# Kernel optimization log

Hardware: AMD Instinct MI355X
Metric: run time of the kernel (lower is better)

The kernel has to match this reference:

```python
import jax, jax.numpy as jnp
import numpy as np

D_MODEL, HEADS, D_FF = 1024, 16, 4096
D_K = D_MODEL // HEADS
EPS = 1e-5


def layer_norm(x, g, b):
    mu = jnp.mean(x, axis=-1, keepdims=True)
    var = jnp.mean((x - mu) ** 2, axis=-1, keepdims=True)
    return (x - mu) * jax.lax.rsqrt(var + EPS) * g + b


def setup_inputs() -> dict:
    key = jax.random.key(0)
    ks = jax.random.split(key, 16)
    B, S = 2, 2048
    s = 0.02
    return {
        "src": jax.random.normal(ks[0], (B, S, D_MODEL), jnp.float32),
        "corr": jax.random.normal(ks[1], (B, S, S), jnp.float32),
        "pos": jax.random.normal(ks[2], (B, S, D_MODEL), jnp.float32),
        "Wq": jax.random.normal(ks[3], (D_MODEL, D_MODEL), jnp.float32) * s,
        "bq": jnp.zeros((D_MODEL,), jnp.float32),
        "Wk": jax.random.normal(ks[4], (D_MODEL, D_MODEL), jnp.float32) * s,
        "bk": jnp.zeros((D_MODEL,), jnp.float32),
        "Wv": jax.random.normal(ks[5], (D_MODEL, D_MODEL), jnp.float32) * s,
        "bv": jnp.zeros((D_MODEL,), jnp.float32),
        "Wo": jax.random.normal(ks[6], (D_MODEL, D_MODEL), jnp.float32) * s,
        "bo": jnp.zeros((D_MODEL,), jnp.float32),
        "W1": jax.random.normal(ks[7], (D_MODEL, D_FF), jnp.float32) * s,
        "b1": jnp.zeros((D_FF,), jnp.float32),
        "W2": jax.random.normal(ks[8], (D_FF, D_MODEL), jnp.float32) * s,
        "b2": jnp.zeros((D_MODEL,), jnp.float32),
        "g1": jnp.ones((D_MODEL,), jnp.float32),
        "be1": jnp.zeros((D_MODEL,), jnp.float32),
        "g2": jnp.ones((D_MODEL,), jnp.float32),
        "be2": jnp.zeros((D_MODEL,), jnp.float32),
    }


def reference(src, corr, pos, Wq, bq, Wk, bk, Wv, bv, Wo, bo, W1, b1, W2, b2, g1, be1, g2, be2):
    B, S, _ = src.shape
    qk_in = src + pos  # with_pos_embed for q and k; value uses raw src
    # QKV projections -> [B, H, S, d_k]
    def split_heads(x):
        return x.reshape(B, S, HEADS, D_K).transpose(0, 2, 1, 3)
    q = split_heads(qk_in @ Wq + bq)
    k = split_heads(qk_in @ Wk + bk)
    v = split_heads(src @ Wv + bv)
    # scores [B, H, S, S] with additive correlation bias before softmax
    scores = jnp.einsum("bhqd,bhkd->bhqk", q, k) / jnp.sqrt(jnp.float32(D_K))
    scores = scores + corr[:, None, :, :]
    attn = jax.nn.softmax(scores, axis=-1)
    ctx = jnp.einsum("bhqk,bhkd->bhqd", attn, v)
    concat = ctx.transpose(0, 2, 1, 3).reshape(B, S, D_MODEL)
    attn_out = concat @ Wo + bo
    # post-norm residual blocks (dropout = identity in eval)
    x = layer_norm(src + attn_out, g1, be1)
    ffn = jax.nn.relu(x @ W1 + b1) @ W2 + b2
    x = layer_norm(x + ffn, g2, be2)
    return x
```

## Files before the change

### kernel.cpp

```cpp
#include <hip/hip_runtime.h>
#include <hip/hip_bf16.h>

#define S_LEN  2048
#define BATCH  2
#define DMODEL 1024
#define NHEAD  16
#define DHEAD  64
#define DFF    4096
#define NTOK   (BATCH * S_LEN)
#define QKVLD  3072

typedef __attribute__((ext_vector_type(8))) short short8;
typedef __attribute__((ext_vector_type(4))) short short4v;
typedef __attribute__((ext_vector_type(4))) float f32x4;

__device__ __forceinline__ short f2bs(float f) {
  __hip_bfloat16 h = __float2bfloat16(f);
  short s;
  __builtin_memcpy(&s, &h, sizeof(short));
  return s;
}

__device__ __forceinline__ float bs2f(short s) {
  unsigned u = ((unsigned)(unsigned short)s) << 16;
  float f;
  __builtin_memcpy(&f, &u, sizeof(float));
  return f;
}

__device__ __forceinline__ f32x4 mfma16(short8 a, short8 b, f32x4 c) {
  return __builtin_amdgcn_mfma_f32_16x16x32_bf16(a, b, c, 0, 0, 0);
}

__device__ __forceinline__ void load_lds16(const short* g, short* l) {
  __builtin_amdgcn_global_load_lds(
      (const __attribute__((address_space(1))) void*)g,
      (__attribute__((address_space(3))) void*)l, 16, 0, 0);
}

__global__ void transpose_cast(const float* __restrict__ in, short* __restrict__ out,
                               int R, int C, float scale) {
  __shared__ float tile[32][33];
  const int c0 = blockIdx.x * 32, r0 = blockIdx.y * 32;
  const int tx = threadIdx.x, ty = threadIdx.y;
#pragma unroll
  for (int i = 0; i < 32; i += 8)
    tile[ty + i][tx] = in[(size_t)(r0 + ty + i) * C + c0 + tx];
  __syncthreads();
#pragma unroll
  for (int i = 0; i < 32; i += 8)
    out[(size_t)(c0 + ty + i) * R + r0 + tx] = f2bs(tile[tx][ty + i] * scale);
}

__global__ __launch_bounds__(256) void transpose_bf16(
    const short* __restrict__ in, short* __restrict__ out, int R, int LDin) {
  __shared__ __attribute__((aligned(16))) short tile[64][72];
  const int c0 = blockIdx.x * 64, r0 = blockIdx.y * 64;
#pragma unroll
  for (int i = 0; i < 2; i++) {
    const int idx = threadIdx.x + 256 * i;
    const int rr = idx >> 3, cc8 = (idx & 7) * 8;
    *(int4*)(&tile[rr][cc8]) = *(const int4*)(in + (size_t)(r0 + rr) * LDin + c0 + cc8);
  }
  __syncthreads();
#pragma unroll
  for (int i = 0; i < 2; i++) {
    const int idx = threadIdx.x + 256 * i;
    const int rr = idx >> 3, cc8 = (idx & 7) * 8;
    short8 v;
#pragma unroll
    for (int j = 0; j < 8; j++) v[j] = tile[cc8 + j][rr];
    *(short8*)(out + (size_t)(c0 + rr) * R + r0 + cc8) = v;
  }
}

__global__ void concat_bias(const float* __restrict__ bq, const float* __restrict__ bk,
                            const float* __restrict__ bv, float* __restrict__ bqkv) {
  const int i = blockIdx.x * 256 + threadIdx.x;
  float v;
  if (i < DMODEL) v = bq[i] * 0.125f;
  else if (i < 2 * DMODEL) v = bk[i - DMODEL];
  else v = bv[i - 2 * DMODEL];
  bqkv[i] = v;
}

__global__ void prep_tokens(const float* __restrict__ src, const float* __restrict__ pos,
                            short* __restrict__ qkb, short* __restrict__ srcb) {
  const int i = (blockIdx.x * blockDim.x + threadIdx.x) * 4;
  float4 s = *(const float4*)(src + i);
  float4 p = *(const float4*)(pos + i);
  short4v q4 = {f2bs(s.x + p.x), f2bs(s.y + p.y), f2bs(s.z + p.z), f2bs(s.w + p.w)};
  short4v s4 = {f2bs(s.x), f2bs(s.y), f2bs(s.z), f2bs(s.w)};
  *(short4v*)(qkb + i) = q4;
  *(short4v*)(srcb + i) = s4;
}

__global__ void prep_corr(const float* __restrict__ corr, short* __restrict__ corrb) {
  const size_t i = ((size_t)blockIdx.x * 256 + threadIdx.x) * 4;
  float4 c = *(const float4*)(corr + i);
  short4v o = {f2bs(c.x), f2bs(c.y), f2bs(c.z), f2bs(c.w)};
  *(short4v*)(corrb + i) = o;
}

template <int RELU, int OUT_BF16>
__global__ __launch_bounds__(256) void gemm_bt(
    const short* __restrict__ A0, const short* __restrict__ A1,
    const short* __restrict__ Bt, const float* __restrict__ bias,
    float* __restrict__ Cf, short* __restrict__ Cb,
    int M, int N, int K, int splitcol) {
  __shared__ __attribute__((aligned(16))) short As[128 * 32];
  __shared__ __attribute__((aligned(16))) short Bs[128 * 32];

  const int tid = threadIdx.x;
  const int wave = tid >> 6, lane = tid & 63;
  const int lm = lane & 15, lq = lane >> 4;
  const int row0 = blockIdx.y * 128, col0 = blockIdx.x * 128;
  const int wr = (wave >> 1) * 64, wc = (wave & 1) * 64;

  const short* A = (col0 < splitcol) ? A0 : A1;
  const short* ag = A + (size_t)(row0 + wave * 32 + (lane >> 2)) * K + (lane & 3) * 8;
  const short* bg = Bt + (size_t)(col0 + wave * 32 + (lane >> 2)) * K + (lane & 3) * 8;
  short* asl = &As[wave * 32 * 32];
  short* bsl = &Bs[wave * 32 * 32];

  f32x4 acc[4][4];
#pragma unroll
  for (int i = 0; i < 4; i++)
#pragma unroll
    for (int j = 0; j < 4; j++) acc[i][j] = (f32x4){0.f, 0.f, 0.f, 0.f};

  for (int k0 = 0; k0 < K; k0 += 32) {
    load_lds16(ag + k0, asl);
    load_lds16(ag + (size_t)16 * K + k0, asl + 16 * 32);
    load_lds16(bg + k0, bsl);
    load_lds16(bg + (size_t)16 * K + k0, bsl + 16 * 32);
    __syncthreads();

    short8 af[4], bfr[4];
#pragma unroll
    for (int i = 0; i < 4; i++)
      af[i] = *(const short8*)(&As[(wr + 16 * i + lm) * 32 + lq * 8]);
#pragma unroll
    for (int j = 0; j < 4; j++)
      bfr[j] = *(const short8*)(&Bs[(wc + 16 * j + lm) * 32 + lq * 8]);
#pragma unroll
    for (int i = 0; i < 4; i++)
#pragma unroll
      for (int j = 0; j < 4; j++) acc[i][j] = mfma16(af[i], bfr[j], acc[i][j]);
    __syncthreads();
  }

#pragma unroll
  for (int i = 0; i < 4; i++) {
#pragma unroll
    for (int j = 0; j < 4; j++) {
      const int col = col0 + wc + 16 * j + lm;
      const float bs = bias[col];
#pragma unroll
      for (int r = 0; r < 4; r++) {
        const int row = row0 + wr + 16 * i + lq * 4 + r;
        float v = acc[i][j][r] + bs;
        if (RELU) v = fmaxf(v, 0.f);
        if (OUT_BF16)
          Cb[(size_t)row * N + col] = f2bs(v);
        else
          Cf[(size_t)row * N + col] = v;
      }
    }
  }
}

__global__ __launch_bounds__(256) void gemm_bt_part(
    const short* __restrict__ A, const short* __restrict__ Bt,
    float* __restrict__ Cf, int M, int N, int K, int Kslice) {
  __shared__ __attribute__((aligned(16))) short As[128 * 32];
  __shared__ __attribute__((aligned(16))) short Bs[128 * 32];

  const int tid = threadIdx.x;
  const int wave = tid >> 6, lane = tid & 63;
  const int lm = lane & 15, lq = lane >> 4;
  const int row0 = blockIdx.y * 128, col0 = blockIdx.x * 128;
  const int kbase = blockIdx.z * Kslice;
  const int wr = (wave >> 1) * 64, wc = (wave & 1) * 64;
  Cf += (size_t)blockIdx.z * M * N;

  const short* ag = A + (size_t)(row0 + wave * 32 + (lane >> 2)) * K + (lane & 3) * 8;
  const short* bg = Bt + (size_t)(col0 + wave * 32 + (lane >> 2)) * K + (lane & 3) * 8;
  short* asl = &As[wave * 32 * 32];
  short* bsl = &Bs[wave * 32 * 32];

  f32x4 acc[4][4];
#pragma unroll
  for (int i = 0; i < 4; i++)
#pragma unroll
    for (int j = 0; j < 4; j++) acc[i][j] = (f32x4){0.f, 0.f, 0.f, 0.f};

  for (int k0 = kbase; k0 < kbase + Kslice; k0 += 32) {
    load_lds16(ag + k0, asl);
    load_lds16(ag + (size_t)16 * K + k0, asl + 16 * 32);
    load_lds16(bg + k0, bsl);
    load_lds16(bg + (size_t)16 * K + k0, bsl + 16 * 32);
    __syncthreads();

    short8 af[4], bfr[4];
#pragma unroll
    for (int i = 0; i < 4; i++)
      af[i] = *(const short8*)(&As[(wr + 16 * i + lm) * 32 + lq * 8]);
#pragma unroll
    for (int j = 0; j < 4; j++)
      bfr[j] = *(const short8*)(&Bs[(wc + 16 * j + lm) * 32 + lq * 8]);
#pragma unroll
    for (int i = 0; i < 4; i++)
#pragma unroll
      for (int j = 0; j < 4; j++) acc[i][j] = mfma16(af[i], bfr[j], acc[i][j]);
    __syncthreads();
  }

#pragma unroll
  for (int i = 0; i < 4; i++) {
#pragma unroll
    for (int j = 0; j < 4; j++) {
      const int col = col0 + wc + 16 * j + lm;
#pragma unroll
      for (int r = 0; r < 4; r++) {
        const int row = row0 + wr + 16 * i + lq * 4 + r;
        Cf[(size_t)row * N + col] = acc[i][j][r];
      }
    }
  }
}

__global__ __launch_bounds__(256, 4) void attn_kernel(
    const short* __restrict__ QKV,
    const short* __restrict__ VT,
    const short* __restrict__ corrb,
    float* __restrict__ Op,
    float* __restrict__ lp) {
  const int h = blockIdx.x, qtile = blockIdx.y;
  const int b = blockIdx.z >> 1, split = blockIdx.z & 1;
  const int koff = split * (S_LEN / 2);
  const int tid = threadIdx.x;
  const int wave = tid >> 6, lane = tid & 63;
  const int lm = lane & 15, lq = lane >> 4;
  const int qb = qtile * 128 + wave * 32;
  const int fx = lm & 7;

  __shared__ __attribute__((aligned(16))) short Ks[64 * 64];
  __shared__ __attribute__((aligned(16))) short Vs[64 * 64];
  __shared__ __attribute__((aligned(16))) short Ps[4 * 32 * 64];

  const short* q0 = QKV + (size_t)(b * S_LEN + qb + lm) * QKVLD + h * DHEAD;
  const short* q1 = q0 + (size_t)16 * QKVLD;
  const short8 qA0 = *(const short8*)(q0 + lq * 8);
  const short8 qA1 = *(const short8*)(q0 + lq * 8 + 32);
  const short8 qB0 = *(const short8*)(q1 + lq * 8);
  const short8 qB1 = *(const short8*)(q1 + lq * 8 + 32);

  f32x4 oA[4], oB[4];
#pragma unroll
  for (int t = 0; t < 4; t++) {
    oA[t] = (f32x4){0.f, 0.f, 0.f, 0.f};
    oB[t] = (f32x4){0.f, 0.f, 0.f, 0.f};
  }
  f32x4 laccA = (f32x4){0.f, 0.f, 0.f, 0.f};
  f32x4 laccB = (f32x4){0.f, 0.f, 0.f, 0.f};

  const short* Kp = QKV + (size_t)(b * S_LEN) * QKVLD + DMODEL + h * DHEAD;
  const short* Vp = VT + (size_t)(h * DHEAD) * NTOK + b * S_LEN;
  const short* c0 = corrb + (size_t)(b * S_LEN + qb + lm) * S_LEN;
  const short* c1 = c0 + (size_t)16 * S_LEN;

  const int sr = tid >> 2;
  const int su = tid & 3;
  const int sw0 = (su ^ (sr & 7)) * 8;
  const int sw1 = ((su + 4) ^ (sr & 7)) * 8;

  for (int kt = koff; kt < koff + S_LEN / 2; kt += 64) {
    const short* kr = Kp + (size_t)(kt + sr) * QKVLD + su * 8;
    const short* vr = Vp + (size_t)sr * NTOK + kt + su * 8;
    *(int4*)(&Ks[sr * 64 + sw0]) = *(const int4*)kr;
    *(int4*)(&Ks[sr * 64 + sw1]) = *(const int4*)(kr + 32);
    *(int4*)(&Vs[sr * 64 + sw0]) = *(const int4*)vr;
    *(int4*)(&Vs[sr * 64 + sw1]) = *(const int4*)(vr + 32);
    __syncthreads();

    f32x4 svA[4], svB[4];
#pragma unroll
    for (int t = 0; t < 4; t++) {
      const int rb = (t * 16 + lm) * 64;
      const short8 kf0 = *(const short8*)(&Ks[rb + (lq ^ fx) * 8]);
      const short8 kf1 = *(const short8*)(&Ks[rb + ((lq + 4) ^ fx) * 8]);
      f32x4 a = (f32x4){0.f, 0.f, 0.f, 0.f};
      a = mfma16(kf0, qA0, a);
      a = mfma16(kf1, qA1, a);
      svA[t] = a;
      f32x4 c = (f32x4){0.f, 0.f, 0.f, 0.f};
      c = mfma16(kf0, qB0, c);
      c = mfma16(kf1, qB1, c);
      svB[t] = c;
    }

#pragma unroll
    for (int t = 0; t < 4; t++) {
      const short4v crA = *(const short4v*)(c0 + kt + t * 16 + lq * 4);
      const short4v crB = *(const short4v*)(c1 + kt + t * 16 + lq * 4);
#pragma unroll
      for (int r = 0; r < 4; r++) {
        svA[t][r] = __expf(svA[t][r] + bs2f(crA[r]));
        svB[t][r] = __expf(svB[t][r] + bs2f(crB[r]));
      }
      laccA += svA[t];
      laccB += svB[t];
      short4v pA = {f2bs(svA[t][0]), f2bs(svA[t][1]), f2bs(svA[t][2]), f2bs(svA[t][3])};
      short4v pB = {f2bs(svB[t][0]), f2bs(svB[t][1]), f2bs(svB[t][2]), f2bs(svB[t][3])};
      const int pu = ((2 * t + (lq >> 1)) ^ fx) * 8 + (lq & 1) * 4;
      *(short4v*)(&Ps[wave * 2048 + lm * 64 + pu]) = pA;
      *(short4v*)(&Ps[wave * 2048 + (16 + lm) * 64 + pu]) = pB;
    }

    const int pbA = wave * 2048 + lm * 64;
    const int pbB = pbA + 16 * 64;
    const short8 pA0 = *(const short8*)(&Ps[pbA + (lq ^ fx) * 8]);
    const short8 pA1 = *(const short8*)(&Ps[pbA + ((lq + 4) ^ fx) * 8]);
    const short8 pB0 = *(const short8*)(&Ps[pbB + (lq ^ fx) * 8]);
    const short8 pB1 = *(const short8*)(&Ps[pbB + ((lq + 4) ^ fx) * 8]);
#pragma unroll
    for (int t = 0; t < 4; t++) {
      const int rb = (t * 16 + lm) * 64;
      const short8 vf0 = *(const short8*)(&Vs[rb + (lq ^ fx) * 8]);
      const short8 vf1 = *(const short8*)(&Vs[rb + ((lq + 4) ^ fx) * 8]);
      oA[t] = mfma16(vf0, pA0, oA[t]);
      oA[t] = mfma16(vf1, pA1, oA[t]);
      oB[t] = mfma16(vf0, pB0, oB[t]);
      oB[t] = mfma16(vf1, pB1, oB[t]);
    }
    __syncthreads();
  }

  float lA = laccA[0] + laccA[1] + laccA[2] + laccA[3];
  float lB = laccB[0] + laccB[1] + laccB[2] + laccB[3];
  lA += __shfl_xor(lA, 16);
  lA += __shfl_xor(lA, 32);
  lB += __shfl_xor(lB, 16);
  lB += __shfl_xor(lB, 32);
  if (lq == 0) {
    lp[((size_t)split * NTOK + b * S_LEN + qb + lm) * NHEAD + h] = lA;
    lp[((size_t)split * NTOK + b * S_LEN + qb + 16 + lm) * NHEAD + h] = lB;
  }
  float* opA = Op + (size_t)split * NTOK * DMODEL +
               (size_t)(b * S_LEN + qb + lm) * DMODEL + h * DHEAD;
  float* opB = opA + (size_t)16 * DMODEL;
#pragma unroll
  for (int t = 0; t < 4; t++) {
    *(f32x4*)(opA + t * 16 + lq * 4) = oA[t];
    *(f32x4*)(opB + t * 16 + lq * 4) = oB[t];
  }
}

__global__ __launch_bounds__(256) void combine_ctx(
    const float* __restrict__ Op, const float* __restrict__ lp,
    short* __restrict__ ctx) {
  const size_t idx = ((size_t)blockIdx.x * 256 + threadIdx.x) * 4;
  const int token = (int)(idx >> 10);
  const int d = (int)(idx & 1023);
  const int h = d >> 6;
  const f32x4 o0 = *(const f32x4*)(Op + idx);
  const f32x4 o1 = *(const f32x4*)(Op + (size_t)NTOK * DMODEL + idx);
  const float l0 = lp[(size_t)token * NHEAD + h];
  const float l1 = lp[((size_t)NTOK + token) * NHEAD + h];
  const float inv = 1.0f / (l0 + l1);
  short4v ov = {f2bs((o0[0] + o1[0]) * inv), f2bs((o0[1] + o1[1]) * inv),
                f2bs((o0[2] + o1[2]) * inv), f2bs((o0[3] + o1[3]) * inv)};
  *(short4v*)(ctx + idx) = ov;
}

__global__ __launch_bounds__(256) void residual_ln3(
    const float* __restrict__ xa, const float* __restrict__ p0,
    const float* __restrict__ p1, const float* __restrict__ bias,
    const float* __restrict__ g, const float* __restrict__ be,
    float* __restrict__ outf, short* __restrict__ outb) {
  const int row = blockIdx.x;
  const int t = threadIdx.x;
  const size_t base = (size_t)row * DMODEL + t * 4;
  float4 a = *(const float4*)(xa + base);
  f32x4 q0 = *(const f32x4*)(p0 + base);
  f32x4 q1 = *(const f32x4*)(p1 + base);
  f32x4 bb = *(const f32x4*)(bias + t * 4);
  const float v0 = a.x + q0[0] + q1[0] + bb[0];
  const float v1 = a.y + q0[1] + q1[1] + bb[1];
  const float v2 = a.z + q0[2] + q1[2] + bb[2];
  const float v3 = a.w + q0[3] + q1[3] + bb[3];
  float sum = v0 + v1 + v2 + v3;
  float sq = v0 * v0 + v1 * v1 + v2 * v2 + v3 * v3;
#pragma unroll
  for (int off = 1; off < 64; off <<= 1) {
    sum += __shfl_xor(sum, off);
    sq += __shfl_xor(sq, off);
  }
  __shared__ float ssum[4], ssq[4];
  const int wave = t >> 6;
  if ((t & 63) == 0) { ssum[wave] = sum; ssq[wave] = sq; }
  __syncthreads();
  sum = ssum[0] + ssum[1] + ssum[2] + ssum[3];
  sq = ssq[0] + ssq[1] + ssq[2] + ssq[3];
  const float mean = sum * (1.0f / DMODEL);
  const float var = sq * (1.0f / DMODEL) - mean * mean;
  const float rstd = rsqrtf(var + 1e-5f);
  float4 gv = *(const float4*)(g + t * 4);
  float4 bv = *(const float4*)(be + t * 4);
  const float o0 = (v0 - mean) * rstd * gv.x + bv.x;
  const float o1 = (v1 - mean) * rstd * gv.y + bv.y;
  const float o2 = (v2 - mean) * rstd * gv.z + bv.z;
  const float o3 = (v3 - mean) * rstd * gv.w + bv.w;
  if (outf) {
    float4 ov = {o0, o1, o2, o3};
    *(float4*)(outf + base) = ov;
  }
  if (outb) {
    short4v ob = {f2bs(o0), f2bs(o1), f2bs(o2), f2bs(o3)};
    *(short4v*)(outb + base) = ob;
  }
}

extern "C" void kernel_launch(void* const* d_in, const int* in_sizes, int n_in,
                              void* d_out, int out_size, void* d_ws, size_t ws_size,
                              hipStream_t stream) {
  const float* src = (const float*)d_in[0];
  const float* corr = (const float*)d_in[1];
  const float* pos = (const float*)d_in[2];
  const float* Wq = (const float*)d_in[3];
  const float* bq = (const float*)d_in[4];
  const float* Wk = (const float*)d_in[5];
  const float* bk = (const float*)d_in[6];
  const float* Wv = (const float*)d_in[7];
  const float* bv = (const float*)d_in[8];
  const float* Wo = (const float*)d_in[9];
  const float* bo = (const float*)d_in[10];
  const float* W1 = (const float*)d_in[11];
  const float* b1 = (const float*)d_in[12];
  const float* W2 = (const float*)d_in[13];
  const float* b2 = (const float*)d_in[14];
  const float* g1 = (const float*)d_in[15];
  const float* be1 = (const float*)d_in[16];
  const float* g2 = (const float*)d_in[17];
  const float* be2 = (const float*)d_in[18];
  float* out = (float*)d_out;

  char* ws = (char*)d_ws;
  size_t off = 0;
  auto alloc = [&](size_t bytes) {
    char* p = ws + off;
    off += (bytes + 255) & ~(size_t)255;
    return p;
  };
  short* WqkvT = (short*)alloc((size_t)QKVLD * DMODEL * 2);
  short* WoT = (short*)alloc((size_t)DMODEL * DMODEL * 2);
  short* W1T = (short*)alloc((size_t)DFF * DMODEL * 2);
  short* W2T = (short*)alloc((size_t)DMODEL * DFF * 2);
  float* bqkv = (float*)alloc((size_t)QKVLD * 4);
  short* qkb = (short*)alloc((size_t)NTOK * DMODEL * 2);
  short* srcb = (short*)alloc((size_t)NTOK * DMODEL * 2);
  short* QKVb = (short*)alloc((size_t)NTOK * QKVLD * 2);
  short* VTt = (short*)alloc((size_t)DMODEL * NTOK * 2);
  short* corrb = (short*)alloc((size_t)BATCH * S_LEN * S_LEN * 2);
  short* ctxb = (short*)alloc((size_t)NTOK * DMODEL * 2);
  float* lp = (float*)alloc((size_t)2 * NTOK * NHEAD * 4);
  float* Pp = (float*)alloc((size_t)2 * NTOK * DMODEL * 4);
  float* x1f = (float*)alloc((size_t)NTOK * DMODEL * 4);
  short* x1b = (short*)alloc((size_t)NTOK * DMODEL * 2);
  short* Hb = (short*)alloc((size_t)NTOK * DFF * 2);
  float* Op = (float*)Hb;

  const dim3 tb(32, 8);
  transpose_cast<<<dim3(32, 32), tb, 0, stream>>>(Wq, WqkvT, DMODEL, DMODEL, 0.125f);
  transpose_cast<<<dim3(32, 32), tb, 0, stream>>>(Wk, WqkvT + (size_t)DMODEL * DMODEL,
                                                  DMODEL, DMODEL, 1.0f);
  transpose_cast<<<dim3(32, 32), tb, 0, stream>>>(Wv, WqkvT + (size_t)2 * DMODEL * DMODEL,
                                                  DMODEL, DMODEL, 1.0f);
  transpose_cast<<<dim3(32, 32), tb, 0, stream>>>(Wo, WoT, DMODEL, DMODEL, 1.0f);
  transpose_cast<<<dim3(128, 32), tb, 0, stream>>>(W1, W1T, DMODEL, DFF, 1.0f);
  transpose_cast<<<dim3(32, 128), tb, 0, stream>>>(W2, W2T, DFF, DMODEL, 1.0f);
  concat_bias<<<QKVLD / 256, 256, 0, stream>>>(bq, bk, bv, bqkv);

  prep_tokens<<<(NTOK * DMODEL) / (256 * 4), 256, 0, stream>>>(src, pos, qkb, srcb);
  prep_corr<<<(BATCH * S_LEN * S_LEN) / (256 * 4), 256, 0, stream>>>(corr, corrb);

  gemm_bt<0, 1><<<dim3(QKVLD / 128, NTOK / 128), 256, 0, stream>>>(
      qkb, srcb, WqkvT, bqkv, nullptr, QKVb, NTOK, QKVLD, DMODEL, 2048);

  transpose_bf16<<<dim3(DMODEL / 64, NTOK / 64), 256, 0, stream>>>(
      QKVb + 2048, VTt, NTOK, QKVLD);

  attn_kernel<<<dim3(NHEAD, S_LEN / 128, BATCH * 2), 256, 0, stream>>>(
      QKVb, VTt, corrb, Op, lp);
  combine_ctx<<<(NTOK * DMODEL) / (256 * 4), 256, 0, stream>>>(Op, lp, ctxb);

  gemm_bt_part<<<dim3(DMODEL / 128, NTOK / 128, 2), 256, 0, stream>>>(
      ctxb, WoT, Pp, NTOK, DMODEL, DMODEL, DMODEL / 2);

  residual_ln3<<<NTOK, 256, 0, stream>>>(src, Pp, Pp + (size_t)NTOK * DMODEL,
                                         bo, g1, be1, x1f, x1b);

  gemm_bt<1, 1><<<dim3(DFF / 128, NTOK / 128), 256, 0, stream>>>(
      x1b, x1b, W1T, b1, nullptr, Hb, NTOK, DFF, DMODEL, 1 << 30);

  gemm_bt_part<<<dim3(DMODEL / 128, NTOK / 128, 2), 256, 0, stream>>>(
      Hb, W2T, Pp, NTOK, DMODEL, DFF, DFF / 2);

  residual_ln3<<<NTOK, 256, 0, stream>>>(x1f, Pp, Pp + (size_t)NTOK * DMODEL,
                                         b2, g2, be2, out, nullptr);
}
```

Baseline: 489.3 us.

## Read fp32 corr directly in attention, split keys four ways, use direct-to-LDS loads

Removes the separate corr-to-bf16 conversion pass and has the attention kernel read the fp32 correlation bias directly, prefetching it before the QK MFMAs. The key dimension is now split four ways instead of two for more blocks, and K/V tiles are staged with direct global-to-LDS loads using an XOR-swizzled layout. MFMA sections get raised wave priority, and the occupancy hint goes from 4 to 5. Partial outputs are placed in the Pp buffer, and the combine kernel sums four partials, which adds more partial-result traffic.

```diff
diff --git a/kernel.cpp b/kernel.cpp
--- a/kernel.cpp
+++ b/kernel.cpp
@@ -9,6 +9,7 @@
 #define DFF    4096
 #define NTOK   (BATCH * S_LEN)
 #define QKVLD  3072
+#define NSPLIT 4
 
 typedef __attribute__((ext_vector_type(8))) short short8;
 typedef __attribute__((ext_vector_type(4))) short short4v;
@@ -93,13 +94,6 @@
   short4v s4 = {f2bs(s.x), f2bs(s.y), f2bs(s.z), f2bs(s.w)};
   *(short4v*)(qkb + i) = q4;
   *(short4v*)(srcb + i) = s4;
-}
-
-__global__ void prep_corr(const float* __restrict__ corr, short* __restrict__ corrb) {
-  const size_t i = ((size_t)blockIdx.x * 256 + threadIdx.x) * 4;
-  float4 c = *(const float4*)(corr + i);
-  short4v o = {f2bs(c.x), f2bs(c.y), f2bs(c.z), f2bs(c.w)};
-  *(short4v*)(corrb + i) = o;
 }
 
 template <int RELU, int OUT_BF16>
@@ -230,15 +224,15 @@
   }
 }
 
-__global__ __launch_bounds__(256, 4) void attn_kernel(
+__global__ __launch_bounds__(256, 5) void attn_kernel(
     const short* __restrict__ QKV,
     const short* __restrict__ VT,
-    const short* __restrict__ corrb,
+    const float* __restrict__ corrf,
     float* __restrict__ Op,
     float* __restrict__ lp) {
   const int h = blockIdx.x, qtile = blockIdx.y;
-  const int b = blockIdx.z >> 1, split = blockIdx.z & 1;
-  const int koff = split * (S_LEN / 2);
+  const int b = blockIdx.z >> 2, split = blockIdx.z & 3;
+  const int koff = split * (S_LEN / NSPLIT);
   const int tid = threadIdx.x;
   const int wave = tid >> 6, lane = tid & 63;
   const int lm = lane & 15, lq = lane >> 4;
@@ -267,24 +261,30 @@
 
   const short* Kp = QKV + (size_t)(b * S_LEN) * QKVLD + DMODEL + h * DHEAD;
   const short* Vp = VT + (size_t)(h * DHEAD) * NTOK + b * S_LEN;
-  const short* c0 = corrb + (size_t)(b * S_LEN + qb + lm) * S_LEN;
-  const short* c1 = c0 + (size_t)16 * S_LEN;
-
-  const int sr = tid >> 2;
-  const int su = tid & 3;
-  const int sw0 = (su ^ (sr & 7)) * 8;
-  const int sw1 = ((su + 4) ^ (sr & 7)) * 8;
-
-  for (int kt = koff; kt < koff + S_LEN / 2; kt += 64) {
-    const short* kr = Kp + (size_t)(kt + sr) * QKVLD + su * 8;
-    const short* vr = Vp + (size_t)sr * NTOK + kt + su * 8;
-    *(int4*)(&Ks[sr * 64 + sw0]) = *(const int4*)kr;
-    *(int4*)(&Ks[sr * 64 + sw1]) = *(const int4*)(kr + 32);
-    *(int4*)(&Vs[sr * 64 + sw0]) = *(const int4*)vr;
-    *(int4*)(&Vs[sr * 64 + sw1]) = *(const int4*)(vr + 32);
+  const float* c0f = corrf + (size_t)(b * S_LEN + qb + lm) * S_LEN;
+  const float* c1f = c0f + (size_t)16 * S_LEN;
+
+  const int srow = wave * 16 + (lane >> 3);
+  const int lu8 = ((lane & 7) ^ (lane >> 3)) * 8;
+  const short* kgA = Kp + (size_t)srow * QKVLD + lu8;
+  const short* vgA = Vp + (size_t)srow * NTOK + lu8;
+
+  for (int kt = koff; kt < koff + S_LEN / NSPLIT; kt += 64) {
+    load_lds16(kgA + (size_t)kt * QKVLD, &Ks[wave * 1024]);
+    load_lds16(kgA + (size_t)(kt + 8) * QKVLD, &Ks[wave * 1024 + 512]);
+    load_lds16(vgA + kt, &Vs[wave * 1024]);
+    load_lds16(vgA + kt + (size_t)8 * NTOK, &Vs[wave * 1024 + 512]);
     __syncthreads();
 
+    f32x4 crA[4], crB[4];
+#pragma unroll
+    for (int t = 0; t < 4; t++) {
+      crA[t] = *(const f32x4*)(c0f + kt + t * 16 + lq * 4);
+      crB[t] = *(const f32x4*)(c1f + kt + t * 16 + lq * 4);
+    }
+
     f32x4 svA[4], svB[4];
+    __builtin_amdgcn_s_setprio(1);
 #pragma unroll
     for (int t = 0; t < 4; t++) {
       const int rb = (t * 16 + lm) * 64;
@@ -299,15 +299,14 @@
       c = mfma16(kf1, qB1, c);
       svB[t] = c;
     }
+    __builtin_amdgcn_s_setprio(0);
 
 #pragma unroll
     for (int t = 0; t < 4; t++) {
-      const short4v crA = *(const short4v*)(c0 + kt + t * 16 + lq * 4);
-      const short4v crB = *(const short4v*)(c1 + kt + t * 16 + lq * 4);
 #pragma unroll
       for (int r = 0; r < 4; r++) {
-        svA[t][r] = __expf(svA[t][r] + bs2f(crA[r]));
-        svB[t][r] = __expf(svB[t][r] + bs2f(crB[r]));
+        svA[t][r] = __expf(svA[t][r] + crA[t][r]);
+        svB[t][r] = __expf(svB[t][r] + crB[t][r]);
       }
       laccA += svA[t];
       laccB += svB[t];
@@ -324,6 +323,7 @@
     const short8 pA1 = *(const short8*)(&Ps[pbA + ((lq + 4) ^ fx) * 8]);
     const short8 pB0 = *(const short8*)(&Ps[pbB + (lq ^ fx) * 8]);
     const short8 pB1 = *(const short8*)(&Ps[pbB + ((lq + 4) ^ fx) * 8]);
+    __builtin_amdgcn_s_setprio(1);
 #pragma unroll
     for (int t = 0; t < 4; t++) {
       const int rb = (t * 16 + lm) * 64;
@@ -334,6 +334,7 @@
       oB[t] = mfma16(vf0, pB0, oB[t]);
       oB[t] = mfma16(vf1, pB1, oB[t]);
     }
+    __builtin_amdgcn_s_setprio(0);
     __syncthreads();
   }
 
@@ -364,13 +365,16 @@
   const int token = (int)(idx >> 10);
   const int d = (int)(idx & 1023);
   const int h = d >> 6;
-  const f32x4 o0 = *(const f32x4*)(Op + idx);
-  const f32x4 o1 = *(const f32x4*)(Op + (size_t)NTOK * DMODEL + idx);
-  const float l0 = lp[(size_t)token * NHEAD + h];
-  const float l1 = lp[((size_t)NTOK + token) * NHEAD + h];
-  const float inv = 1.0f / (l0 + l1);
-  short4v ov = {f2bs((o0[0] + o1[0]) * inv), f2bs((o0[1] + o1[1]) * inv),
-                f2bs((o0[2] + o1[2]) * inv), f2bs((o0[3] + o1[3]) * inv)};
+  f32x4 o = (f32x4){0.f, 0.f, 0.f, 0.f};
+  float l = 0.f;
+#pragma unroll
+  for (int s = 0; s < NSPLIT; s++) {
+    o += *(const f32x4*)(Op + (size_t)s * NTOK * DMODEL + idx);
+    l += lp[((size_t)s * NTOK + token) * NHEAD + h];
+  }
+  const float inv = 1.0f / l;
+  short4v ov = {f2bs(o[0] * inv), f2bs(o[1] * inv),
+                f2bs(o[2] * inv), f2bs(o[3] * inv)};
   *(short4v*)(ctx + idx) = ov;
 }
 
@@ -462,14 +466,13 @@
   short* srcb = (short*)alloc((size_t)NTOK * DMODEL * 2);
   short* QKVb = (short*)alloc((size_t)NTOK * QKVLD * 2);
   short* VTt = (short*)alloc((size_t)DMODEL * NTOK * 2);
-  short* corrb = (short*)alloc((size_t)BATCH * S_LEN * S_LEN * 2);
   short* ctxb = (short*)alloc((size_t)NTOK * DMODEL * 2);
-  float* lp = (float*)alloc((size_t)2 * NTOK * NHEAD * 4);
+  float* lp = (float*)alloc((size_t)NSPLIT * NTOK * NHEAD * 4);
   float* Pp = (float*)alloc((size_t)2 * NTOK * DMODEL * 4);
+  short* Hb = (short*)alloc((size_t)NTOK * DFF * 2);
+  float* Op = Pp;
   float* x1f = (float*)alloc((size_t)NTOK * DMODEL * 4);
   short* x1b = (short*)alloc((size_t)NTOK * DMODEL * 2);
-  short* Hb = (short*)alloc((size_t)NTOK * DFF * 2);
-  float* Op = (float*)Hb;
 
   const dim3 tb(32, 8);
   transpose_cast<<<dim3(32, 32), tb, 0, stream>>>(Wq, WqkvT, DMODEL, DMODEL, 0.125f);
@@ -483,7 +486,6 @@
   concat_bias<<<QKVLD / 256, 256, 0, stream>>>(bq, bk, bv, bqkv);
 
   prep_tokens<<<(NTOK * DMODEL) / (256 * 4), 256, 0, stream>>>(src, pos, qkb, srcb);
-  prep_corr<<<(BATCH * S_LEN * S_LEN) / (256 * 4), 256, 0, stream>>>(corr, corrb);
 
   gemm_bt<0, 1><<<dim3(QKVLD / 128, NTOK / 128), 256, 0, stream>>>(
       qkb, srcb, WqkvT, bqkv, nullptr, QKVb, NTOK, QKVLD, DMODEL, 2048);
@@ -491,8 +493,8 @@
   transpose_bf16<<<dim3(DMODEL / 64, NTOK / 64), 256, 0, stream>>>(
       QKVb + 2048, VTt, NTOK, QKVLD);
 
-  attn_kernel<<<dim3(NHEAD, S_LEN / 128, BATCH * 2), 256, 0, stream>>>(
-      QKVb, VTt, corrb, Op, lp);
+  attn_kernel<<<dim3(NHEAD, S_LEN / 128, BATCH * NSPLIT), 256, 0, stream>>>(
+      QKVb, VTt, corr, Op, lp);
   combine_ctx<<<(NTOK * DMODEL) / (256 * 4), 256, 0, stream>>>(Op, lp, ctxb);
 
   gemm_bt_part<<<dim3(DMODEL / 128, NTOK / 128, 2), 256, 0, stream>>>(
```

After: 760.5 us. 55.4% more time.
